# Kernel tuning notes

Measured on AMD Instinct MI355X. Metric: run time of the kernel, lower is better.

## Reference

```python
import jax, jax.numpy as jnp
import numpy as np

# Static problem sizes
B, TMAX = 32, 48                 # subjects, max windows per subject
NPW, NWIN = 128, 1024            # nodes per window, total windows (= sum(lengths))
EPW = 2048                       # edges per window (avg degree 16)
N, E = NWIN * NPW, NWIN * EPW    # 131072 nodes, 2097152 edges
IN_DIM, GNN_H, GRU_H = 128, 128, 128


def setup_inputs() -> dict:
    key = jax.random.key(0)
    ks = jax.random.split(key, 12)
    x = jax.random.normal(ks[0], (N, IN_DIM), jnp.float32)
    # random intra-window edges: endpoints within each window's 128-node block
    base = jax.random.randint(ks[1], (2, NWIN, EPW), 0, NPW)
    offs = (jnp.arange(NWIN) * NPW)[None, :, None]
    edge_index = (base + offs).reshape(2, E)
    batch_idx = jnp.repeat(jnp.arange(NWIN), NPW)          # node -> window id
    lengths = jnp.asarray(np.tile([16, 48], B // 2), jnp.int32)  # sums to NWIN
    s = 0.05
    p = lambda k, shape: jax.random.normal(k, shape, jnp.float32) * s
    return dict(
        x=x, edge_index=edge_index, batch_idx=batch_idx, lengths=lengths,
        # GIN layer 1 MLP (weights stored [in,out])
        w1a=p(ks[2], (IN_DIM, GNN_H)), b1a=jnp.zeros((GNN_H,), jnp.float32),
        w1b=p(ks[3], (GNN_H, GNN_H)), b1b=jnp.zeros((GNN_H,), jnp.float32),
        # GIN layer 2 MLP
        w2a=p(ks[4], (GNN_H, GNN_H)), b2a=jnp.zeros((GNN_H,), jnp.float32),
        w2b=p(ks[5], (GNN_H, GNN_H)), b2b=jnp.zeros((GNN_H,), jnp.float32),
        # GRU (torch layout: [3H, in], gate order r,z,n)
        wih=p(ks[6], (3 * GRU_H, GNN_H)), whh=p(ks[7], (3 * GRU_H, GRU_H)),
        bih=jnp.zeros((3 * GRU_H,), jnp.float32), bhh=jnp.zeros((3 * GRU_H,), jnp.float32),
        # output head
        wout=p(ks[8], (GRU_H, 1)), bout=jnp.zeros((1,), jnp.float32),
    )


def _gin(h, src, dst, wa, ba, wb, bb):
    # GINConv with eps=0: mlp(x + sum_{j->i} x_j)
    aggr = jax.ops.segment_sum(h[src], dst, num_segments=N)
    z = h + aggr
    z = jax.nn.relu(z @ wa + ba)
    return z @ wb + bb


def _forward(x, w1a, b1a, w1b, b1b, w2a, b2a, w2b, b2b,
             wih, whh, bih, bhh, wout, bout, edge_index, batch_idx, lengths):
    src, dst = edge_index[0], edge_index[1]
    h = jax.nn.relu(_gin(x, src, dst, w1a, b1a, w1b, b1b))
    h = jax.nn.relu(_gin(h, src, dst, w2a, b2a, w2b, b2b))
    # global mean pool per window -> [NWIN, GNN_H]
    sums = jax.ops.segment_sum(h, batch_idx, num_segments=NWIN)
    cnt = jax.ops.segment_sum(jnp.ones((N, 1), h.dtype), batch_idx, num_segments=NWIN)
    g = sums / cnt
    # pad_sequence: scatter flat window embeddings into [B, TMAX, H]
    csum = jnp.cumsum(lengths)
    starts = jnp.concatenate([jnp.zeros((1,), lengths.dtype), csum[:-1]])
    win_ids = jnp.arange(NWIN)
    subj = jnp.searchsorted(csum, win_ids, side='right')
    pos = win_ids - starts[subj]
    padded = jnp.zeros((B, TMAX, GNN_H), g.dtype).at[subj, pos].set(g)
    # masked GRU == pack_padded_sequence semantics (state frozen past length)
    mask = jnp.arange(TMAX)[:, None] < lengths[None, :]   # [T, B]
    xs = jnp.swapaxes(padded, 0, 1)                        # [T, B, H]

    def step(hc, inputs):
        xt, mt = inputs
        gx = xt @ wih.T + bih
        gh = hc @ whh.T + bhh
        rx, zx, nx = jnp.split(gx, 3, axis=-1)
        rh, zh, nh = jnp.split(gh, 3, axis=-1)
        r = jax.nn.sigmoid(rx + rh)
        z = jax.nn.sigmoid(zx + zh)
        n = jnp.tanh(nx + r * nh)
        hn = (1 - z) * n + z * hc
        hn = jnp.where(mt[:, None], hn, hc)
        return hn, None

    h0 = jnp.zeros((B, GRU_H), g.dtype)
    h_last, _ = jax.lax.scan(step, h0, (xs, mask))
    return (h_last @ wout + bout).squeeze(-1)  # [B]


def reference(x, edge_index, batch_idx, lengths,
              w1a, b1a, w1b, b1b, w2a, b2a, w2b, b2b,
              wih, whh, bih, bhh, wout, bout):
    return _forward(x, w1a, b1a, w1b, b1b, w2a, b2a, w2b, b2b,
                    wih, whh, bih, bhh, wout, bout, edge_index, batch_idx, lengths)
```

## Files before the change

kernel.cpp:

```cpp
#include <hip/hip_runtime.h>
#include <hip/hip_bf16.h>
#include <stdint.h>

#define NPW   128
#define NWIN  1024
#define EPW   2048
#define NEDGE (NWIN * EPW)
#define BSUBJ 32
#define TMAXW 48

typedef __bf16 bf16x8_t __attribute__((ext_vector_type(8)));
typedef float  f32x4_t  __attribute__((ext_vector_type(4)));

#define MU4_OFF  0
#define B2_OFF   8192
#define B3_OFF   40960
#define BIAS_OFF 73728
#define GP_OFF   75776
#define META_OFF 76288
#define K1_LDS   76800

__device__ __forceinline__ unsigned short bfbits(float v) {
  return __builtin_bit_cast(unsigned short, (__bf16)v);
}
__device__ __forceinline__ int swz(int row, int colbyte) {
  return row * 256 + (colbyte ^ ((row & 15) << 4));
}

__device__ __forceinline__ void gemm_lds(const char* Ab, const char* Bb, int lane, int rt,
                                         f32x4_t acc[8]) {
  const int rowA = rt * 16 + (lane & 15);
  const int swA = (rowA & 15) << 4;
  const int swB = (lane & 15) << 4;
  #pragma unroll
  for (int kk = 0; kk < 4; ++kk) {
    const int kb = kk * 64 + (lane >> 4) * 16;
    bf16x8_t af = *(const bf16x8_t*)(Ab + rowA * 256 + (kb ^ swA));
    #pragma unroll
    for (int ct = 0; ct < 8; ++ct) {
      const int rowB = ct * 16 + (lane & 15);
      bf16x8_t bv = *(const bf16x8_t*)(Bb + rowB * 256 + (kb ^ swB));
      acc[ct] = __builtin_amdgcn_mfma_f32_16x16x32_bf16(af, bv, acc[ct], 0, 0, 0);
    }
  }
}

__device__ __forceinline__ void gemm_m(const unsigned* Mw, const char* Bb, int lane, int rt,
                                       f32x4_t acc[8]) {
  const int rowA = rt * 16 + (lane & 15);
  const int g = lane >> 4;
  const int swB = (lane & 15) << 4;
  #pragma unroll
  for (int kk = 0; kk < 4; ++kk) {
    const unsigned mw = Mw[rowA * 16 + ((kk * 4 + g) ^ (rowA & 15))];
    bf16x8_t af;
    #pragma unroll
    for (int e = 0; e < 8; ++e)
      af[e] = (__bf16)(float)((mw >> (4 * e)) & 15u);
    const int kb = kk * 64 + g * 16;
    #pragma unroll
    for (int ct = 0; ct < 8; ++ct) {
      const int rowB = ct * 16 + (lane & 15);
      bf16x8_t bv = *(const bf16x8_t*)(Bb + rowB * 256 + (kb ^ swB));
      acc[ct] = __builtin_amdgcn_mfma_f32_16x16x32_bf16(af, bv, acc[ct], 0, 0, 0);
    }
  }
}

__device__ __forceinline__ void write_row(char* Dst, int lane, int rt, const f32x4_t acc[8],
                                          const float* bias, bool relu) {
  const int r0 = rt * 16 + (lane >> 4) * 4;
  const int c = lane & 15;
  #pragma unroll
  for (int ct = 0; ct < 8; ++ct) {
    const int col = ct * 16 + c;
    const float bvl = bias ? bias[col] : 0.f;
    #pragma unroll
    for (int j = 0; j < 4; ++j) {
      float v = acc[ct][j] + bvl;
      if (relu) v = fmaxf(v, 0.f);
      *(__bf16*)(Dst + swz(r0 + j, col * 2)) = (__bf16)v;
    }
  }
}

__device__ __forceinline__ void write_tr(char* Dst, int lane, int rt, const f32x4_t acc[8],
                                         const float* bias, bool relu) {
  const int r0 = rt * 16 + (lane >> 4) * 4;
  const int c = lane & 15;
  #pragma unroll
  for (int ct = 0; ct < 8; ++ct) {
    const int col = ct * 16 + c;
    const float bvl = bias ? bias[col] : 0.f;
    unsigned long long pk = 0ull;
    #pragma unroll
    for (int j = 0; j < 4; ++j) {
      float v = acc[ct][j] + bvl;
      if (relu) v = fmaxf(v, 0.f);
      pk |= ((unsigned long long)bfbits(v)) << (16 * j);
    }
    *(unsigned long long*)(Dst + swz(col, r0 * 2)) = pk;
  }
}

__device__ __forceinline__ void wload(const char* src, int tid, float4 wr[4]) {
  #pragma unroll
  for (int p = 0; p < 4; ++p)
    wr[p] = *(const float4*)(src + p * 8192 + tid * 16);
}
__device__ __forceinline__ void wstore(char* B3, int tid, const float4 wr[4]) {
  #pragma unroll
  for (int p = 0; p < 4; ++p)
    *(float4*)(B3 + p * 8192 + tid * 16) = wr[p];
}

__global__ void __launch_bounds__(128)
wprep_kernel(const float* __restrict__ w1a, const float* __restrict__ w1b,
             const float* __restrict__ w2a, const float* __restrict__ w2b,
             unsigned* __restrict__ wt) {
  const float* srcs[4] = {w1a, w1b, w2a, w2b};
  const float* src = srcs[blockIdx.x];
  const int j = threadIdx.x;
  unsigned* dst = wt + blockIdx.x * 8192 + j * 64;
  const int sw = (j & 15) << 2;
  #pragma unroll 8
  for (int k = 0; k < 64; ++k) {
    float a = src[(size_t)(2 * k) * 128 + j];
    float b = src[(size_t)(2 * k + 1) * 128 + j];
    dst[k ^ sw] = (unsigned)bfbits(a) | ((unsigned)bfbits(b) << 16);
  }
}

__global__ void __launch_bounds__(512, 4)
gin_gnn_kernel(const float* __restrict__ x, const int* __restrict__ ei,
               const float* __restrict__ b1a, const float* __restrict__ b1b,
               const float* __restrict__ b2a, const float* __restrict__ b2b,
               const char* __restrict__ wt_sw, const float* __restrict__ wih,
               const float* __restrict__ bih, const int* __restrict__ lengths,
               float* __restrict__ GX) {
  extern __shared__ __align__(16) char sm[];
  const int w = blockIdx.x;
  const int tid = threadIdx.x;
  const int lane = tid & 63;
  const int wv = tid >> 6;

  unsigned* Mw = (unsigned*)(sm + MU4_OFF);
  char* B2 = sm + B2_OFF;
  char* B3 = sm + B3_OFF;
  float* biasb = (float*)(sm + BIAS_OFF);
  float* gp = (float*)(sm + GP_OFF);
  int* meta = (int*)(sm + META_OFF);

  #pragma unroll
  for (int i = tid; i < 2048; i += 512) Mw[i] = 0u;
  if (tid < 128) gp[tid] = 0.f;
  __syncthreads();

  if (tid < 64) {
    int L = (tid < BSUBJ) ? lengths[tid] : 0;
    int c = L;
    #pragma unroll
    for (int d = 1; d < 32; d <<= 1) {
      int u = __shfl_up(c, d, 64);
      if (tid >= d) c += u;
    }
    unsigned long long mset = __ballot(tid < BSUBJ && w < c);
    int s = (int)(__ffsll((long long)mset) - 1);
    if (tid == s) { meta[0] = s; meta[1] = w - (c - L); }
  }
  {
    const int base = w * EPW;
    #pragma unroll
    for (int rr = 0; rr < 4; ++rr) {
      const int e = base + tid + rr * 512;
      const int s = ei[e] & 127;
      const int d = ei[NEDGE + e] & 127;
      atomicAdd(&Mw[d * 16 + ((s >> 3) ^ (d & 15))], 1u << ((s & 7) * 4));
    }
    if (tid < 128) {
      const int d = tid;
      atomicAdd(&Mw[d * 16 + ((d >> 3) ^ (d & 15))], 1u << ((d & 7) * 4));
    }
  }
  {
    const int i0 = (tid & 63) * 2, f0 = (tid >> 6) * 16;
    const float* r0p = x + ((size_t)w * 128 + i0) * 128 + f0;
    const float* r1p = r0p + 128;
    float va[16], vb[16];
    #pragma unroll
    for (int c = 0; c < 4; ++c) {
      *(float4*)(va + 4 * c) = *(const float4*)(r0p + 4 * c);
      *(float4*)(vb + 4 * c) = *(const float4*)(r1p + 4 * c);
    }
    #pragma unroll
    for (int q = 0; q < 16; ++q) {
      const int f = f0 + q;
      unsigned pk = (unsigned)bfbits(va[q]) | ((unsigned)bfbits(vb[q]) << 16);
      *(unsigned*)(B2 + f * 256 + ((4 * (tid & 63)) ^ ((f & 15) << 4))) = pk;
    }
  }
  {
    const float* bp = (tid < 128) ? b1a : (tid < 256) ? b1b : (tid < 384) ? b2a : b2b;
    biasb[tid] = bp[tid & 127];
  }
  float4 wr[4];
  wload(wt_sw, tid, wr);
  wstore(B3, tid, wr);
  __syncthreads();

  f32x4_t acc[8];
  #define ZACC() { _Pragma("unroll") for (int q = 0; q < 8; ++q) acc[q] = (f32x4_t){0.f,0.f,0.f,0.f}; }

  ZACC(); gemm_m(Mw, B2, lane, wv, acc);
  wload(wt_sw + 32768, tid, wr);
  __syncthreads();
  write_row(B2, lane, wv, acc, nullptr, false);
  __syncthreads();
  ZACC(); gemm_lds(B2, B3, lane, wv, acc);
  __syncthreads();
  write_row(B2, lane, wv, acc, biasb + 0, true);
  wstore(B3, tid, wr);
  wload(wt_sw + 65536, tid, wr);
  __syncthreads();
  ZACC(); gemm_lds(B2, B3, lane, wv, acc);
  __syncthreads();
  write_tr(B2, lane, wv, acc, biasb + 128, true);
  wstore(B3, tid, wr);
  wload(wt_sw + 98304, tid, wr);
  __syncthreads();
  ZACC(); gemm_m(Mw, B2, lane, wv, acc);
  __syncthreads();
  write_row(B2, lane, wv, acc, nullptr, false);
  __syncthreads();
  ZACC(); gemm_lds(B2, B3, lane, wv, acc);
  __syncthreads();
  write_row(B2, lane, wv, acc, biasb + 256, true);
  wstore(B3, tid, wr);
  __syncthreads();
  ZACC(); gemm_lds(B2, B3, lane, wv, acc);
  {
    const int c = lane & 15;
    #pragma unroll
    for (int ct = 0; ct < 8; ++ct) {
      const int col = ct * 16 + c;
      const float bvl = biasb[384 + col];
      float s = 0.f;
      #pragma unroll
      for (int j = 0; j < 4; ++j) s += fmaxf(acc[ct][j] + bvl, 0.f);
      s += __shfl_xor(s, 16);
      s += __shfl_xor(s, 32);
      if (lane < 16) atomicAdd(&gp[col], s);
    }
  }
  __syncthreads();

  if (tid < 384) {
    const float* wrow = wih + (size_t)tid * 128;
    const float4* gp4 = (const float4*)gp;
    float a0 = 0.f, a1 = 0.f, a2 = 0.f, a3 = 0.f;
    #pragma unroll
    for (int q = 0; q < 8; ++q) {
      const float4 h0 = gp4[4*q], h1 = gp4[4*q+1], h2 = gp4[4*q+2], h3 = gp4[4*q+3];
      const float4 w0 = *(const float4*)(wrow + 16*q);
      const float4 w1 = *(const float4*)(wrow + 16*q + 4);
      const float4 w2 = *(const float4*)(wrow + 16*q + 8);
      const float4 w3 = *(const float4*)(wrow + 16*q + 12);
      a0 = fmaf(w0.x,h0.x,fmaf(w0.y,h0.y,fmaf(w0.z,h0.z,fmaf(w0.w,h0.w,a0))));
      a1 = fmaf(w1.x,h1.x,fmaf(w1.y,h1.y,fmaf(w1.z,h1.z,fmaf(w1.w,h1.w,a1))));
      a2 = fmaf(w2.x,h2.x,fmaf(w2.y,h2.y,fmaf(w2.z,h2.z,fmaf(w2.w,h2.w,a2))));
      a3 = fmaf(w3.x,h3.x,fmaf(w3.y,h3.y,fmaf(w3.z,h3.z,fmaf(w3.w,h3.w,a3))));
    }
    const float dot = (a0 + a1) + (a2 + a3);
    GX[((size_t)meta[0] * TMAXW + meta[1]) * 384 + tid] = dot * (1.f / 128.f) + bih[tid];
  }
}

__global__ void __launch_bounds__(384)
gru_kernel(const float* __restrict__ GX, const float* __restrict__ whh,
           const float* __restrict__ bhh, const float* __restrict__ wout,
           const float* __restrict__ bout, const int* __restrict__ lengths,
           float* __restrict__ outp) {
  __shared__ __align__(16) float hb[128];
  __shared__ float rb[128], zb[128];
  const int b = blockIdx.x;
  const int o = threadIdx.x;

  float wrf[128];
  {
    const float* wr = whh + (size_t)o * 128;
    #pragma unroll
    for (int q = 0; q < 32; ++q) {
      float4 v = ((const float4*)wr)[q];
      wrf[4*q+0] = v.x; wrf[4*q+1] = v.y; wrf[4*q+2] = v.z; wrf[4*q+3] = v.w;
    }
  }
  if (o < 128) hb[o] = 0.f;
  const float bho = bhh[o];
  const int len = lengths[b];
  __syncthreads();

  float gx = (len > 0) ? GX[((size_t)b * TMAXW) * 384 + o] : 0.f;
  for (int t = 0; t < len; ++t) {
    const int tn = (t + 1 < len) ? t + 1 : t;
    const float gxn = GX[((size_t)b * TMAXW + tn) * 384 + o];
    float a0 = 0.f, a1 = 0.f, a2 = 0.f, a3 = 0.f;
    const float4* hv4 = (const float4*)hb;
    #pragma unroll
    for (int q = 0; q < 8; ++q) {
      const float4 h0 = hv4[4*q], h1 = hv4[4*q+1], h2 = hv4[4*q+2], h3 = hv4[4*q+3];
      const float* wq = wrf + 16 * q;
      a0 = fmaf(wq[0],  h0.x, a0); a0 = fmaf(wq[1],  h0.y, a0);
      a0 = fmaf(wq[2],  h0.z, a0); a0 = fmaf(wq[3],  h0.w, a0);
      a1 = fmaf(wq[4],  h1.x, a1); a1 = fmaf(wq[5],  h1.y, a1);
      a1 = fmaf(wq[6],  h1.z, a1); a1 = fmaf(wq[7],  h1.w, a1);
      a2 = fmaf(wq[8],  h2.x, a2); a2 = fmaf(wq[9],  h2.y, a2);
      a2 = fmaf(wq[10], h2.z, a2); a2 = fmaf(wq[11], h2.w, a2);
      a3 = fmaf(wq[12], h3.x, a3); a3 = fmaf(wq[13], h3.y, a3);
      a3 = fmaf(wq[14], h3.z, a3); a3 = fmaf(wq[15], h3.w, a3);
    }
    const float gh = (a0 + a1) + (a2 + a3) + bho;
    float nsave = 0.f, ghn = 0.f;
    if (o < 256) {
      const float v = 1.f / (1.f + __expf(-(gx + gh)));
      if (o < 128) rb[o] = v; else zb[o - 128] = v;
    } else {
      nsave = gx; ghn = gh;
    }
    __syncthreads();
    if (o >= 256) {
      const int oo = o - 256;
      const float r = rb[oo], z = zb[oo];
      const float pre = nsave + r * ghn;
      const float e2 = __expf(-2.f * pre);
      const float n = (1.f - e2) / (1.f + e2);
      hb[oo] = (1.f - z) * n + z * hb[oo];
    }
    __syncthreads();
    gx = gxn;
  }

  float part = (o < 128) ? hb[o] * wout[o] : 0.f;
  #pragma unroll
  for (int d = 1; d < 64; d <<= 1) part += __shfl_xor(part, d);
  __shared__ float red[6];
  if ((o & 63) == 0) red[o >> 6] = part;
  __syncthreads();
  if (o == 0) outp[b] = red[0] + red[1] + bout[0];
}

extern "C" void kernel_launch(void* const* d_in, const int* in_sizes, int n_in,
                              void* d_out, int out_size, void* d_ws, size_t ws_size,
                              hipStream_t stream) {
  const float* x    = (const float*)d_in[0];
  const int*   ei   = (const int*)d_in[1];
  const int*   len  = (const int*)d_in[3];
  const float* w1a  = (const float*)d_in[4];
  const float* b1a  = (const float*)d_in[5];
  const float* w1b  = (const float*)d_in[6];
  const float* b1b  = (const float*)d_in[7];
  const float* w2a  = (const float*)d_in[8];
  const float* b2a  = (const float*)d_in[9];
  const float* w2b  = (const float*)d_in[10];
  const float* b2b  = (const float*)d_in[11];
  const float* wih  = (const float*)d_in[12];
  const float* whh  = (const float*)d_in[13];
  const float* bih  = (const float*)d_in[14];
  const float* bhh  = (const float*)d_in[15];
  const float* wout = (const float*)d_in[16];
  const float* bout = (const float*)d_in[17];

  float*    GX    = (float*)d_ws;
  unsigned* wt_sw = (unsigned*)((char*)d_ws + (size_t)BSUBJ * TMAXW * 384 * 4);

  hipLaunchKernelGGL(wprep_kernel, dim3(4), dim3(128), 0, stream,
                     w1a, w1b, w2a, w2b, wt_sw);
  hipLaunchKernelGGL(gin_gnn_kernel, dim3(NWIN), dim3(512), K1_LDS, stream,
                     x, ei, b1a, b1b, b2a, b2b, (const char*)wt_sw,
                     wih, bih, len, GX);
  hipLaunchKernelGGL(gru_kernel, dim3(BSUBJ), dim3(384), 0, stream,
                     GX, whh, bhh, wout, bout, len, (float*)d_out);
}
```

Before: 283.7 us.

## Reorder GIN as (A+I)(XW) and stage weights via direct global-to-LDS loads

Uses associativity to compute X·W first and then apply the adjacency (A+I) matrix, so each layer runs one GEMM and one aggregation with the transpose written once. The input load becomes a row-major coalesced float4 read, and weight tiles are staged straight into LDS with global_load_lds instead of passing through registers. The aim is to cut register pressure, barriers and redundant LDS writes. Launch bounds drop from 4 to 2 blocks per SM, which allows more registers but lowers the occupancy hint. Rounding to bf16 now happens at different points, which can shift numerics slightly.

```diff
diff --git a/kernel.cpp b/kernel.cpp
--- a/kernel.cpp
+++ b/kernel.cpp
@@ -27,6 +27,16 @@
   return row * 256 + (colbyte ^ ((row & 15) << 4));
 }
 
+#define GLDS16(gaddr, laddr) __builtin_amdgcn_global_load_lds( \
+    (const __attribute__((address_space(1))) unsigned*)(gaddr), \
+    (__attribute__((address_space(3))) unsigned*)(laddr), 16, 0, 0)
+
+__device__ __forceinline__ void wstage(const char* src, char* dstB3, int wv, int lane) {
+  #pragma unroll
+  for (int p = 0; p < 4; ++p)
+    GLDS16(src + wv * 4096 + p * 1024 + lane * 16, dstB3 + wv * 4096 + p * 1024);
+}
+
 __device__ __forceinline__ void gemm_lds(const char* Ab, const char* Bb, int lane, int rt,
                                          f32x4_t acc[8]) {
   const int rowA = rt * 16 + (lane & 15);
@@ -101,17 +111,6 @@
     }
     *(unsigned long long*)(Dst + swz(col, r0 * 2)) = pk;
   }
-}
-
-__device__ __forceinline__ void wload(const char* src, int tid, float4 wr[4]) {
-  #pragma unroll
-  for (int p = 0; p < 4; ++p)
-    wr[p] = *(const float4*)(src + p * 8192 + tid * 16);
-}
-__device__ __forceinline__ void wstore(char* B3, int tid, const float4 wr[4]) {
-  #pragma unroll
-  for (int p = 0; p < 4; ++p)
-    *(float4*)(B3 + p * 8192 + tid * 16) = wr[p];
 }
 
 __global__ void __launch_bounds__(128)
@@ -131,7 +130,7 @@
   }
 }
 
-__global__ void __launch_bounds__(512, 4)
+__global__ void __launch_bounds__(512, 2)
 gin_gnn_kernel(const float* __restrict__ x, const int* __restrict__ ei,
                const float* __restrict__ b1a, const float* __restrict__ b1b,
                const float* __restrict__ b2a, const float* __restrict__ b2b,
@@ -156,6 +155,7 @@
   if (tid < 128) gp[tid] = 0.f;
   __syncthreads();
 
+  wstage(wt_sw, B3, wv, lane);
   if (tid < 64) {
     int L = (tid < BSUBJ) ? lengths[tid] : 0;
     int c = L;
@@ -183,59 +183,51 @@
     }
   }
   {
-    const int i0 = (tid & 63) * 2, f0 = (tid >> 6) * 16;
-    const float* r0p = x + ((size_t)w * 128 + i0) * 128 + f0;
-    const float* r1p = r0p + 128;
-    float va[16], vb[16];
-    #pragma unroll
-    for (int c = 0; c < 4; ++c) {
-      *(float4*)(va + 4 * c) = *(const float4*)(r0p + 4 * c);
-      *(float4*)(vb + 4 * c) = *(const float4*)(r1p + 4 * c);
-    }
-    #pragma unroll
-    for (int q = 0; q < 16; ++q) {
-      const int f = f0 + q;
-      unsigned pk = (unsigned)bfbits(va[q]) | ((unsigned)bfbits(vb[q]) << 16);
-      *(unsigned*)(B2 + f * 256 + ((4 * (tid & 63)) ^ ((f & 15) << 4))) = pk;
+    const float* xw = x + (size_t)w * 16384;
+    #pragma unroll
+    for (int it = 0; it < 8; ++it) {
+      const int elem = it * 2048 + tid * 4;
+      const float4 v = *(const float4*)(xw + elem);
+      const int row = elem >> 7;
+      const int colb = (elem & 127) * 2;
+      unsigned long long pk = (unsigned long long)bfbits(v.x)
+          | ((unsigned long long)bfbits(v.y) << 16)
+          | ((unsigned long long)bfbits(v.z) << 32)
+          | ((unsigned long long)bfbits(v.w) << 48);
+      *(unsigned long long*)(B2 + row * 256 + (colb ^ ((row & 15) << 4))) = pk;
     }
   }
   {
     const float* bp = (tid < 128) ? b1a : (tid < 256) ? b1b : (tid < 384) ? b2a : b2b;
     biasb[tid] = bp[tid & 127];
   }
-  float4 wr[4];
-  wload(wt_sw, tid, wr);
-  wstore(B3, tid, wr);
   __syncthreads();
 
   f32x4_t acc[8];
   #define ZACC() { _Pragma("unroll") for (int q = 0; q < 8; ++q) acc[q] = (f32x4_t){0.f,0.f,0.f,0.f}; }
 
+  ZACC(); gemm_lds(B2, B3, lane, wv, acc);
+  __syncthreads();
+  write_tr(B2, lane, wv, acc, nullptr, false);
+  wstage(wt_sw + 32768, B3, wv, lane);
+  __syncthreads();
   ZACC(); gemm_m(Mw, B2, lane, wv, acc);
-  wload(wt_sw + 32768, tid, wr);
-  __syncthreads();
-  write_row(B2, lane, wv, acc, nullptr, false);
+  __syncthreads();
+  write_row(B2, lane, wv, acc, biasb + 0, true);
   __syncthreads();
   ZACC(); gemm_lds(B2, B3, lane, wv, acc);
   __syncthreads();
-  write_row(B2, lane, wv, acc, biasb + 0, true);
-  wstore(B3, tid, wr);
-  wload(wt_sw + 65536, tid, wr);
+  write_row(B2, lane, wv, acc, biasb + 128, true);
+  wstage(wt_sw + 65536, B3, wv, lane);
   __syncthreads();
   ZACC(); gemm_lds(B2, B3, lane, wv, acc);
   __syncthreads();
-  write_tr(B2, lane, wv, acc, biasb + 128, true);
-  wstore(B3, tid, wr);
-  wload(wt_sw + 98304, tid, wr);
+  write_tr(B2, lane, wv, acc, nullptr, false);
+  wstage(wt_sw + 98304, B3, wv, lane);
   __syncthreads();
   ZACC(); gemm_m(Mw, B2, lane, wv, acc);
   __syncthreads();
-  write_row(B2, lane, wv, acc, nullptr, false);
-  __syncthreads();
-  ZACC(); gemm_lds(B2, B3, lane, wv, acc);
-  __syncthreads();
   write_row(B2, lane, wv, acc, biasb + 256, true);
-  wstore(B3, tid, wr);
   __syncthreads();
   ZACC(); gemm_lds(B2, B3, lane, wv, acc);
   {
```

Result: faster. 256.9 us (-9.4%).
